# Kernel tuning notes

Measured on AMD Instinct MI355X. Metric: run time of the kernel, lower is better.

The kernel has to match this reference:

```python
import jax, jax.numpy as jnp
import numpy as np
from jax import lax

KSIZE = 3
STRIDE = 1
RATE = 2
FUSE_K = 3
SCALE = 10.0
DN = ('NCHW', 'OIHW', 'NCHW')


def _same_pad_amount(size, k, s):
    out = (size + s - 1) // s
    pad = max(0, (out - 1) * s + k - size)
    return pad // 2, pad - pad // 2


def extract_patches(x, k, s):
    # torch.nn.Unfold with 'same' padding; returns [B, L, C, k, k], L row-major
    B, C, H, W = x.shape
    pt, pb = _same_pad_amount(H, k, s)
    pl, pr = _same_pad_amount(W, k, s)
    xp = jnp.pad(x, ((0, 0), (0, 0), (pt, pb), (pl, pr)))
    Ho = (H + s - 1) // s
    Wo = (W + s - 1) // s
    rows = (jnp.arange(Ho) * s)[:, None] + jnp.arange(k)[None, :]  # [Ho,k]
    cols = (jnp.arange(Wo) * s)[:, None] + jnp.arange(k)[None, :]  # [Wo,k]
    p = xp[:, :, rows, :][:, :, :, :, cols]  # [B,C,Ho,k,Wo,k]
    return p.transpose(0, 2, 4, 1, 3, 5).reshape(B, Ho * Wo, C, k, k)


def setup_inputs() -> dict:
    key = jax.random.key(0)
    kf, kb = jax.random.split(key)
    f = jax.random.normal(kf, (2, 128, 128, 128), dtype=jnp.float32)
    b = jax.random.normal(kb, (2, 128, 128, 128), dtype=jnp.float32)
    mask = jnp.zeros((1, 1, 128, 128), dtype=jnp.float32)  # all patches available
    return {"f": f, "b": b, "mask": mask}


def reference(f, b, mask):
    B, C, Hr, Wr = f.shape
    kernel = 2 * RATE
    # raw background patches for final aggregation: [B, Lb, C, 4, 4]
    raw_w = extract_patches(b, kernel, RATE * STRIDE)
    # nearest downsample by rate (src_idx = i*rate)
    f_ds = f[:, :, ::RATE, ::RATE]
    b_ds = b[:, :, ::RATE, ::RATE]
    Hf, Wf = f_ds.shape[2], f_ds.shape[3]
    Hb, Wb = b_ds.shape[2], b_ds.shape[3]
    L = Hb * Wb
    # matching patches: [B, L, C, 3, 3]
    w = extract_patches(b_ds, KSIZE, STRIDE)
    # mask patches (shared across batch, torch uses m[0])
    m_ds = mask[:, :, ::RATE, ::RATE]
    m = extract_patches(m_ds, KSIZE, STRIDE)[0]  # [L,1,3,3]
    mm = (jnp.mean(m, axis=(1, 2, 3)) == 0.0).astype(f.dtype).reshape(1, L, 1, 1)
    # L2-normalize patch filters (escape_NaN added elementwise before sum, as in torch)
    wn = w / jnp.sqrt(jnp.sum(w * w + 1e-4, axis=(2, 3, 4), keepdims=True))

    def score_one(xi, wi):
        # xi [C,Hf,Wf], wi [L,C,3,3] -> [L,Hf,Wf]
        return lax.conv_general_dilated(xi[None], wi, (1, 1), [(1, 1), (1, 1)],
                                        dimension_numbers=DN)[0]

    y = jax.vmap(score_one)(f_ds, wn)  # [B, L, Hf, Wf]

    # diagonal fuse: identity 3x3 conv on the [L, Hf*Wf] score matrix, twice with transpose
    fw = jnp.eye(FUSE_K, dtype=f.dtype).reshape(1, 1, FUSE_K, FUSE_K)

    def fuse_conv(t):
        return lax.conv_general_dilated(t, fw, (1, 1), [(1, 1), (1, 1)],
                                        dimension_numbers=DN)

    y = y.reshape(B, 1, Hb * Wb, Hf * Wf)
    y = fuse_conv(y).reshape(B, Hb, Wb, Hf, Wf)
    y = y.transpose(0, 2, 1, 4, 3).reshape(B, 1, L, Hf * Wf)
    y = fuse_conv(y).reshape(B, Wb, Hb, Wf, Hf)
    y = y.transpose(0, 2, 1, 4, 3).reshape(B, L, Hf, Wf)

    y = y * mm
    y = jax.nn.softmax(y * SCALE, axis=1) * mm

    def deconv_one(a, wc):
        # conv_transpose2d(a, wc, stride=rate, padding=1); wc [L,C,4,4]
        wt = jnp.flip(wc, (-2, -1)).transpose(1, 0, 2, 3)  # [C,L,4,4]
        pad = kernel - 1 - 1
        return lax.conv_general_dilated(a[None], wt, (1, 1), [(pad, pad), (pad, pad)],
                                        lhs_dilation=(RATE, RATE),
                                        dimension_numbers=DN)[0]

    out = jax.vmap(deconv_one)(y, raw_w) / 4.0  # [B, C, Hr, Wr]
    return out
```

## Files before the change

kernel.cpp:

```cpp
#include <hip/hip_runtime.h>
#include <cstdint>

typedef _Float16 f16x8 __attribute__((ext_vector_type(8)));
typedef float f32x4 __attribute__((ext_vector_type(4)));

typedef __attribute__((address_space(1))) void gvoid;
typedef __attribute__((address_space(3))) void lvoid;

__device__ __forceinline__ void gload16(const void* g, void* l) {
    __builtin_amdgcn_global_load_lds((gvoid*)g, (lvoid*)l, 16, 0, 0);
}

__device__ __forceinline__ void bar() {
    asm volatile("" ::: "memory");
    __builtin_amdgcn_s_barrier();
    asm volatile("" ::: "memory");
}
#define WAITV(N) asm volatile("s_waitcnt vmcnt(" #N ")" ::: "memory")

__global__ __launch_bounds__(256) void downsample_kernel(const float* __restrict__ f,
                                                         const float* __restrict__ b,
                                                         float* __restrict__ fds,
                                                         float* __restrict__ bds) {
    int idx = blockIdx.x * 256 + threadIdx.x;
    const float* src = blockIdx.y ? b : f;
    float* dst = blockIdx.y ? bds : fds;
    int bb = idx >> 19;
    int r = idx & 524287;
    int c = r >> 12, a = (r >> 6) & 63, v = r & 63;
    dst[idx] = src[(size_t)bb * 2097152 + (size_t)c * 16384 + (2 * a) * 128 + 2 * v];
}

__global__ __launch_bounds__(256) void build_mm_kernel(const float* __restrict__ mask,
                                                       float* __restrict__ mm) {
    int l = blockIdx.x * 256 + threadIdx.x;
    if (l >= 4096) return;
    int i = l >> 6, j = l & 63;
    float s = 0.f;
    #pragma unroll
    for (int dy = 0; dy < 3; ++dy)
        #pragma unroll
        for (int dx = 0; dx < 3; ++dx) {
            int a = i + dy - 1, b = j + dx - 1;
            if ((unsigned)a < 64u && (unsigned)b < 64u)
                s += mask[(2 * a) * 128 + 2 * b];
        }
    mm[l] = (s == 0.0f) ? 1.0f : 0.0f;
}

__global__ __launch_bounds__(256) void build_fpatch_kernel(const float* __restrict__ fds,
                                                           _Float16* __restrict__ Fp) {
    int bb = blockIdx.x >> 12;
    int p = blockIdx.x & 4095;
    const float* fb = fds + (size_t)bb * 524288;
    _Float16* Fpb = Fp + (size_t)bb * 4718592;
    int u = p >> 6, v = p & 63;
    for (int k = threadIdx.x; k < 1152; k += 256) {
        int c = k / 9;
        int s = k - 9 * c;
        int dy = s / 3, dx = s - 3 * dy;
        int a = u + dy - 1, bcol = v + dx - 1;
        float val = 0.f;
        if ((unsigned)a < 64u && (unsigned)bcol < 64u)
            val = fb[c * 4096 + a * 64 + bcol];
        Fpb[(size_t)p * 1152 + k] = (_Float16)val;
    }
}

__global__ __launch_bounds__(256) void build_wn_kernel(const float* __restrict__ bds,
                                                       _Float16* __restrict__ Wn) {
    __shared__ float wsh[1152];
    __shared__ float red[4];
    int bb = blockIdx.x >> 12;
    int l = blockIdx.x & 4095;
    const float* bp = bds + (size_t)bb * 524288;
    _Float16* Wnb = Wn + (size_t)bb * 4718592;
    int i = l >> 6, j = l & 63;
    float sq = 0.f;
    for (int k = threadIdx.x; k < 1152; k += 256) {
        int c = k / 9;
        int s = k - 9 * c;
        int dy = s / 3, dx = s - 3 * dy;
        int a = i + dy - 1, bcol = j + dx - 1;
        float val = 0.f;
        if ((unsigned)a < 64u && (unsigned)bcol < 64u)
            val = bp[c * 4096 + a * 64 + bcol];
        wsh[k] = val;
        sq += val * val;
    }
    #pragma unroll
    for (int off = 32; off > 0; off >>= 1) sq += __shfl_xor(sq, off);
    if ((threadIdx.x & 63) == 0) red[threadIdx.x >> 6] = sq;
    __syncthreads();
    float total = red[0] + red[1] + red[2] + red[3] + 0.1152f;
    float rinv = 1.0f / sqrtf(total);
    for (int k = threadIdx.x; k < 1152; k += 256)
        Wnb[(size_t)l * 1152 + k] = (_Float16)(wsh[k] * rinv);
}

__global__ __launch_bounds__(256) void build_vt_kernel(const float* __restrict__ b,
                                                       _Float16* __restrict__ Vt) {
    int bb = blockIdx.x >> 11;
    int n = blockIdx.x & 2047;
    const float* bp = b + (size_t)bb * 2097152;
    _Float16* Vtb = Vt + (size_t)bb * 8388608;
    int c = n >> 4, r = n & 15, rh = r >> 2, rw = r & 3;
    const float* bc = bp + (size_t)c * 16384;
    for (int l = threadIdx.x; l < 4096; l += 256) {
        int lh = l >> 6, lw = l & 63;
        int row = 2 * lh + rh - 1, col = 2 * lw + rw - 1;
        float val = 0.f;
        if ((unsigned)row < 128u && (unsigned)col < 128u)
            val = bc[row * 128 + col];
        Vtb[(size_t)n * 4096 + l] = (_Float16)val;
    }
}

template <int KSTR, int NTILES>
__device__ __forceinline__ void gemm_core(const _Float16* __restrict__ A,
                                          const _Float16* __restrict__ Bt,
                                          _Float16* __restrict__ C,
                                          _Float16* __restrict__ AsB,
                                          _Float16* __restrict__ BsB) {
    const int tid = threadIdx.x;
    const int lane = tid & 63;
    const int wave = tid >> 6;
    const int quad = lane >> 4;
    const int l16 = lane & 15;
    const int wm = wave >> 2;
    const int wn = wave & 3;
    const int bm = blockIdx.y * 256;
    const int bn = blockIdx.x * 256;

    f32x4 acc[8][4] = {};
    f16x8 afr[2][4], bfr[2][4];

    const int s0 = tid, s1 = 512 + tid;
    const int sr0 = s0 >> 2, sr1 = s1 >> 2;
    const int r0 = sr0 ^ ((sr0 >> 2) & 1);
    const int r1 = sr1 ^ ((sr1 >> 2) & 1);
    const int q0 = (s0 & 3) ^ (r0 & 3);
    const int q1 = (s1 & 3) ^ (r1 & 3);
    const int offA0 = (bm + r0) * KSTR + q0 * 8;
    const int offA1 = (bm + r1) * KSTR + q1 * 8;
    const int offB0 = (bn + r0) * KSTR + q0 * 8;
    const int offB1 = (bn + r1) * KSTR + q1 * 8;

#define STAGE_A(buf, kt, kh) do {                                                          \
        gload16(A + offA0 + (kt) * 64 + (kh) * 32, AsB + ((buf) * 2 + (kh)) * 8192 + tid * 8); \
        gload16(A + offA1 + (kt) * 64 + (kh) * 32, AsB + ((buf) * 2 + (kh)) * 8192 + 4096 + tid * 8); \
    } while (0)
#define STAGE_B(buf, kt, kh) do {                                                          \
        gload16(Bt + offB0 + (kt) * 64 + (kh) * 32, BsB + ((buf) * 2 + (kh)) * 8192 + tid * 8); \
        gload16(Bt + offB1 + (kt) * 64 + (kh) * 32, BsB + ((buf) * 2 + (kh)) * 8192 + 4096 + tid * 8); \
    } while (0)

    const int c2 = (l16 >> 2) & 1;
    const int rdoff = ((l16 ^ c2) * 32) + ((quad ^ (l16 & 3)) * 8);

#define LDA(par, buf, kh, mh) do {                                                         \
        _Pragma("unroll")                                                                  \
        for (int mi = 0; mi < 4; ++mi)                                                     \
            afr[par][mi] = *(const f16x8*)&AsB[((buf) * 2 + (kh)) * 8192 +                 \
                (wm * 128 + ((mh) * 4 + mi) * 16) * 32 + rdoff];                           \
    } while (0)
#define LDB(par, buf, kh) do {                                                             \
        _Pragma("unroll")                                                                  \
        for (int ni = 0; ni < 4; ++ni)                                                     \
            bfr[par][ni] = *(const f16x8*)&BsB[((buf) * 2 + (kh)) * 8192 +                 \
                (wn * 64 + ni * 16) * 32 + rdoff];                                         \
    } while (0)
#define MM(apar, bpar, mh) do {                                                            \
        __builtin_amdgcn_s_setprio(1);                                                     \
        _Pragma("unroll")                                                                  \
        for (int mi = 0; mi < 4; ++mi)                                                     \
            _Pragma("unroll")                                                              \
            for (int ni = 0; ni < 4; ++ni)                                                 \
                acc[(mh) * 4 + mi][ni] = __builtin_amdgcn_mfma_f32_16x16x32_f16(           \
                    afr[apar][mi], bfr[bpar][ni], acc[(mh) * 4 + mi][ni], 0, 0, 0);        \
        __builtin_amdgcn_s_setprio(0);                                                     \
    } while (0)

    STAGE_A(0, 0, 0); STAGE_B(0, 0, 0);
    STAGE_A(0, 0, 1); STAGE_B(0, 0, 1);
    STAGE_A(1, 1, 0); STAGE_B(1, 1, 0);
    WAITV(4);
    bar();
    LDA(0, 0, 0, 0); LDB(0, 0, 0);

    #pragma unroll 1
    for (int i = 0; i < NTILES / 2 - 1; ++i) {
        const int t0 = 2 * i;
        STAGE_A(1, t0 + 1, 1); bar();
        LDA(1, 0, 0, 1); MM(0, 0, 0); bar();
        STAGE_B(1, t0 + 1, 1); bar();
        LDA(0, 0, 1, 0); LDB(1, 0, 1); MM(1, 0, 1); bar();
        STAGE_A(0, t0 + 2, 0); bar();
        LDA(1, 0, 1, 1); MM(0, 1, 0); bar();
        STAGE_B(0, t0 + 2, 0); WAITV(4); bar();
        LDA(0, 1, 0, 0); LDB(0, 1, 0); MM(1, 1, 1); bar();
        STAGE_A(0, t0 + 2, 1); bar();
        LDA(1, 1, 0, 1); MM(0, 0, 0); bar();
        STAGE_B(0, t0 + 2, 1); bar();
        LDA(0, 1, 1, 0); LDB(1, 1, 1); MM(1, 0, 1); bar();
        STAGE_A(1, t0 + 3, 0); bar();
        LDA(1, 1, 1, 1); MM(0, 1, 0); bar();
        STAGE_B(1, t0 + 3, 0); WAITV(4); bar();
        LDA(0, 0, 0, 0); LDB(0, 0, 0); MM(1, 1, 1); bar();
    }

    STAGE_A(1, NTILES - 1, 1); bar();
    LDA(1, 0, 0, 1); MM(0, 0, 0); bar();
    STAGE_B(1, NTILES - 1, 1); bar();
    LDA(0, 0, 1, 0); LDB(1, 0, 1); MM(1, 0, 1); bar();
    LDA(1, 0, 1, 1); MM(0, 1, 0); bar();
    WAITV(0); bar();
    LDA(0, 1, 0, 0); LDB(0, 1, 0); MM(1, 1, 1); bar();
    LDA(1, 1, 0, 1); MM(0, 0, 0); bar();
    LDA(0, 1, 1, 0); LDB(1, 1, 1); MM(1, 0, 1); bar();
    LDA(1, 1, 1, 1); MM(0, 1, 0); bar();
    MM(1, 1, 1);

#undef STAGE_A
#undef STAGE_B
#undef LDA
#undef LDB
#undef MM

    #pragma unroll
    for (int mi = 0; mi < 8; ++mi)
        #pragma unroll
        for (int ni = 0; ni < 4; ++ni)
            #pragma unroll
            for (int r = 0; r < 4; ++r) {
                int row = bm + wm * 128 + mi * 16 + quad * 4 + r;
                int col = bn + wn * 64 + ni * 16 + l16;
                C[(size_t)row * 4096 + col] = (_Float16)acc[mi][ni][r];
            }
}

__global__ __launch_bounds__(512, 2) void gemm1_kernel(const _Float16* __restrict__ Fp,
                                                       const _Float16* __restrict__ Wn,
                                                       _Float16* __restrict__ S0) {
    __shared__ __align__(16) _Float16 As[2][2][8192];
    __shared__ __align__(16) _Float16 Bs[2][2][8192];
    const int z = blockIdx.z;
    gemm_core<1152, 18>(Fp + (size_t)z * 4718592, Wn + (size_t)z * 4718592,
                        S0 + (size_t)z * 16777216, &As[0][0][0], &Bs[0][0][0]);
}

__global__ __launch_bounds__(512, 2) void gemm2_kernel(const _Float16* __restrict__ Vt,
                                                       const _Float16* __restrict__ att0,
                                                       const _Float16* __restrict__ att1,
                                                       _Float16* __restrict__ OTh) {
    __shared__ __align__(16) _Float16 As[2][2][8192];
    __shared__ __align__(16) _Float16 Bs[2][2][8192];
    const int z = blockIdx.z;
    gemm_core<4096, 64>(Vt + (size_t)z * 8388608, z ? att1 : att0,
                        OTh + (size_t)z * 8388608, &As[0][0][0], &Bs[0][0][0]);
}

__global__ __launch_bounds__(256) void fuse_softmax_kernel(const _Float16* __restrict__ S0,
                                                           const float* __restrict__ mm,
                                                           _Float16* __restrict__ att0,
                                                           _Float16* __restrict__ att1) {
    __shared__ float red[4];
    const int tid = threadIdx.x;
    const int lane = tid & 63;
    const int wave = tid >> 6;
    int g = blockIdx.x;
    int p_global = ((g & 7) << 10) | (g >> 3);
    const int bb = p_global >> 12;
    const int p = p_global & 4095;
    const _Float16* S = S0 + (size_t)bb * 16777216;
    _Float16* att = bb ? att1 : att0;
    const int pbase = ((p & 63) << 6) | (p >> 6);

    float acc[16];
    #pragma unroll
    for (int k = 0; k < 16; ++k) acc[k] = 0.f;

    #pragma unroll
    for (int t2 = -1; t2 <= 1; ++t2) {
        int b2 = pbase + t2;
        if ((unsigned)b2 >= 4096u) continue;
        int pp = ((b2 & 63) << 6) | (b2 >> 6);
        #pragma unroll
        for (int t1 = -1; t1 <= 1; ++t1) {
            int rr = pp + t1;
            if ((unsigned)rr >= 4096u) continue;
            const _Float16* row = S + (size_t)rr * 4096;
            #pragma unroll
            for (int k = 0; k < 16; ++k) {
                int l = k * 256 + tid;
                int i = (k * 256 + wave * 64) >> 6;
                int it2 = i + t2;
                if (it2 >= 0 && it2 < 64) {
                    int c = l + t2 * 64 + t1;
                    if ((unsigned)c < 4096u)
                        acc[k] += (float)row[c];
                } else if (it2 == 64) {
                    if (lane <= 62) {
                        int c = lane + 1 + t1;
                        if ((unsigned)c < 4096u) acc[k] += (float)row[c];
                    }
                } else {
                    if (lane >= 1) {
                        int c = 4031 + lane + t1;
                        if ((unsigned)c < 4096u) acc[k] += (float)row[c];
                    }
                }
            }
        }
    }

    float mv[16];
    float lmax = -1e30f;
    #pragma unroll
    for (int k = 0; k < 16; ++k) {
        int l = k * 256 + tid;
        mv[k] = mm[l];
        float lg = acc[k] * mv[k] * 10.0f;
        acc[k] = lg;
        lmax = fmaxf(lmax, lg);
    }
    #pragma unroll
    for (int off = 32; off > 0; off >>= 1) lmax = fmaxf(lmax, __shfl_xor(lmax, off));
    if (lane == 0) red[wave] = lmax;
    __syncthreads();
    lmax = fmaxf(fmaxf(red[0], red[1]), fmaxf(red[2], red[3]));
    __syncthreads();

    float lsum = 0.f;
    #pragma unroll
    for (int k = 0; k < 16; ++k) {
        float e = __expf(acc[k] - lmax);
        acc[k] = e;
        lsum += e;
    }
    #pragma unroll
    for (int off = 32; off > 0; off >>= 1) lsum += __shfl_xor(lsum, off);
    if (lane == 0) red[wave] = lsum;
    __syncthreads();
    float inv = 1.0f / (red[0] + red[1] + red[2] + red[3]);
    #pragma unroll
    for (int k = 0; k < 16; ++k) {
        int l = k * 256 + tid;
        att[(size_t)p * 4096 + l] = (_Float16)(acc[k] * inv * mv[k]);
    }
}

__global__ __launch_bounds__(256) void assemble_kernel(const _Float16* __restrict__ OTh,
                                                       float* __restrict__ out) {
    int idx = blockIdx.x * 256 + threadIdx.x;
    int bb = idx >> 21;
    int w = idx & 2097151;
    const _Float16* OTb = OTh + (size_t)bb * 8388608;
    int x = w & 127, y = (w >> 7) & 127, c = w >> 14;
    int r0 = (y + 1) & 1, s0 = (x + 1) & 1;
    float acc = 0.f;
    #pragma unroll
    for (int a = 0; a < 2; ++a) {
        int rh = r0 + 2 * a;
        int ph = (y + 1 - rh) >> 1;
        if ((unsigned)ph < 64u) {
            #pragma unroll
            for (int bq = 0; bq < 2; ++bq) {
                int rw = s0 + 2 * bq;
                int pw = (x + 1 - rw) >> 1;
                if ((unsigned)pw < 64u)
                    acc += (float)OTb[(size_t)(c * 16 + rh * 4 + rw) * 4096 + ph * 64 + pw];
            }
        }
    }
    out[idx] = 0.25f * acc;
}

extern "C" void kernel_launch(void* const* d_in, const int* in_sizes, int n_in,
                              void* d_out, int out_size, void* d_ws, size_t ws_size,
                              hipStream_t stream) {
    const float* f = (const float*)d_in[0];
    const float* b = (const float*)d_in[1];
    const float* mask = (const float*)d_in[2];
    float* out = (float*)d_out;
    char* ws = (char*)d_ws;

    float* mm = (float*)ws;
    _Float16* Fp = (_Float16*)(ws + 16384);
    _Float16* Wn = (_Float16*)(ws + 16384 + 18874368);
    _Float16* att0 = (_Float16*)(ws + 16384);
    _Float16* S0 = (_Float16*)(ws + 37765120);
    _Float16* Vt = (_Float16*)(ws + 37765120);
    _Float16* OTh = (_Float16*)(ws + 37765120 + 33554432);
    float* fds = (float*)(ws + 104873984);
    float* bds = (float*)(ws + 104873984 + 4194304);
    _Float16* att1 = (_Float16*)(ws + 104873984);

    downsample_kernel<<<dim3(4096, 2), 256, 0, stream>>>(f, b, fds, bds);
    build_mm_kernel<<<16, 256, 0, stream>>>(mask, mm);
    build_fpatch_kernel<<<8192, 256, 0, stream>>>(fds, Fp);
    build_wn_kernel<<<8192, 256, 0, stream>>>(bds, Wn);

    gemm1_kernel<<<dim3(16, 16, 2), 512, 0, stream>>>(Fp, Wn, S0);
    fuse_softmax_kernel<<<8192, 256, 0, stream>>>(S0, mm, att0, att1);

    build_vt_kernel<<<4096, 256, 0, stream>>>(b, Vt);
    gemm2_kernel<<<dim3(16, 8, 2), 512, 0, stream>>>(Vt, att0, att1, OTh);
    assemble_kernel<<<16384, 256, 0, stream>>>(OTh, out);
}
```

Before: 431.1 us.

## Replace double-buffered register fragments with single-buffered loads and explicit LDS waits

```diff
diff --git a/kernel.cpp b/kernel.cpp
--- a/kernel.cpp
+++ b/kernel.cpp
@@ -17,6 +17,8 @@
     asm volatile("" ::: "memory");
 }
 #define WAITV(N) asm volatile("s_waitcnt vmcnt(" #N ")" ::: "memory")
+#define WAITL0 do { asm volatile("s_waitcnt lgkmcnt(0)" ::: "memory"); \
+                    __builtin_amdgcn_sched_barrier(0); } while (0)
 
 __global__ __launch_bounds__(256) void downsample_kernel(const float* __restrict__ f,
                                                          const float* __restrict__ b,
@@ -133,7 +135,6 @@
     const int bn = blockIdx.x * 256;
 
     f32x4 acc[8][4] = {};
-    f16x8 afr[2][4], bfr[2][4];
 
     const int s0 = tid, s1 = 512 + tid;
     const int sr0 = s0 >> 2, sr1 = s1 >> 2;
@@ -158,74 +159,72 @@
     const int c2 = (l16 >> 2) & 1;
     const int rdoff = ((l16 ^ c2) * 32) + ((quad ^ (l16 & 3)) * 8);
 
-#define LDA(par, buf, kh, mh) do {                                                         \
-        _Pragma("unroll")                                                                  \
-        for (int mi = 0; mi < 4; ++mi)                                                     \
-            afr[par][mi] = *(const f16x8*)&AsB[((buf) * 2 + (kh)) * 8192 +                 \
-                (wm * 128 + ((mh) * 4 + mi) * 16) * 32 + rdoff];                           \
-    } while (0)
-#define LDB(par, buf, kh) do {                                                             \
-        _Pragma("unroll")                                                                  \
-        for (int ni = 0; ni < 4; ++ni)                                                     \
-            bfr[par][ni] = *(const f16x8*)&BsB[((buf) * 2 + (kh)) * 8192 +                 \
-                (wn * 64 + ni * 16) * 32 + rdoff];                                         \
-    } while (0)
-#define MM(apar, bpar, mh) do {                                                            \
-        __builtin_amdgcn_s_setprio(1);                                                     \
-        _Pragma("unroll")                                                                  \
-        for (int mi = 0; mi < 4; ++mi)                                                     \
-            _Pragma("unroll")                                                              \
-            for (int ni = 0; ni < 4; ++ni)                                                 \
-                acc[(mh) * 4 + mi][ni] = __builtin_amdgcn_mfma_f32_16x16x32_f16(           \
-                    afr[apar][mi], bfr[bpar][ni], acc[(mh) * 4 + mi][ni], 0, 0, 0);        \
-        __builtin_amdgcn_s_setprio(0);                                                     \
-    } while (0)
+    f16x8 afr[4], bfr[4];
+    auto LDA = [&](int buf, int kh, int mh) {
+        #pragma unroll
+        for (int mi = 0; mi < 4; ++mi)
+            afr[mi] = *(const f16x8*)&AsB[((buf) * 2 + (kh)) * 8192 +
+                                          (wm * 128 + ((mh) * 4 + mi) * 16) * 32 + rdoff];
+    };
+    auto LDB = [&](int buf, int kh) {
+        #pragma unroll
+        for (int ni = 0; ni < 4; ++ni)
+            bfr[ni] = *(const f16x8*)&BsB[((buf) * 2 + (kh)) * 8192 +
+                                          (wn * 64 + ni * 16) * 32 + rdoff];
+    };
+    auto MM = [&](int mh) {
+        __builtin_amdgcn_s_setprio(1);
+        #pragma unroll
+        for (int mi = 0; mi < 4; ++mi)
+            #pragma unroll
+            for (int ni = 0; ni < 4; ++ni)
+                acc[mh * 4 + mi][ni] = __builtin_amdgcn_mfma_f32_16x16x32_f16(
+                    afr[mi], bfr[ni], acc[mh * 4 + mi][ni], 0, 0, 0);
+        __builtin_amdgcn_s_setprio(0);
+    };
 
     STAGE_A(0, 0, 0); STAGE_B(0, 0, 0);
     STAGE_A(0, 0, 1); STAGE_B(0, 0, 1);
     STAGE_A(1, 1, 0); STAGE_B(1, 1, 0);
     WAITV(4);
     bar();
-    LDA(0, 0, 0, 0); LDB(0, 0, 0);
 
     #pragma unroll 1
     for (int i = 0; i < NTILES / 2 - 1; ++i) {
         const int t0 = 2 * i;
-        STAGE_A(1, t0 + 1, 1); bar();
-        LDA(1, 0, 0, 1); MM(0, 0, 0); bar();
-        STAGE_B(1, t0 + 1, 1); bar();
-        LDA(0, 0, 1, 0); LDB(1, 0, 1); MM(1, 0, 1); bar();
-        STAGE_A(0, t0 + 2, 0); bar();
-        LDA(1, 0, 1, 1); MM(0, 1, 0); bar();
-        STAGE_B(0, t0 + 2, 0); WAITV(4); bar();
-        LDA(0, 1, 0, 0); LDB(0, 1, 0); MM(1, 1, 1); bar();
-        STAGE_A(0, t0 + 2, 1); bar();
-        LDA(1, 1, 0, 1); MM(0, 0, 0); bar();
-        STAGE_B(0, t0 + 2, 1); bar();
-        LDA(0, 1, 1, 0); LDB(1, 1, 1); MM(1, 0, 1); bar();
-        STAGE_A(1, t0 + 3, 0); bar();
-        LDA(1, 1, 1, 1); MM(0, 1, 0); bar();
-        STAGE_B(1, t0 + 3, 0); WAITV(4); bar();
-        LDA(0, 0, 0, 0); LDB(0, 0, 0); MM(1, 1, 1); bar();
-    }
-
-    STAGE_A(1, NTILES - 1, 1); bar();
-    LDA(1, 0, 0, 1); MM(0, 0, 0); bar();
-    STAGE_B(1, NTILES - 1, 1); bar();
-    LDA(0, 0, 1, 0); LDB(1, 0, 1); MM(1, 0, 1); bar();
-    LDA(1, 0, 1, 1); MM(0, 1, 0); bar();
-    WAITV(0); bar();
-    LDA(0, 1, 0, 0); LDB(0, 1, 0); MM(1, 1, 1); bar();
-    LDA(1, 1, 0, 1); MM(0, 0, 0); bar();
-    LDA(0, 1, 1, 0); LDB(1, 1, 1); MM(1, 0, 1); bar();
-    LDA(1, 1, 1, 1); MM(0, 1, 0); bar();
-    MM(1, 1, 1);
+        LDA(0, 0, 0); LDB(0, 0); STAGE_A(1, t0 + 1, 1);
+        bar(); WAITL0; MM(0); bar();
+        LDA(0, 0, 1); STAGE_B(1, t0 + 1, 1);
+        bar(); WAITL0; MM(1); bar();
+        LDA(0, 1, 0); LDB(0, 1); STAGE_A(0, t0 + 2, 0);
+        bar(); WAITL0; MM(0); bar();
+        LDA(0, 1, 1); STAGE_B(0, t0 + 2, 0); WAITV(4);
+        bar(); WAITL0; MM(1); bar();
+        LDA(1, 0, 0); LDB(1, 0); STAGE_A(0, t0 + 2, 1);
+        bar(); WAITL0; MM(0); bar();
+        LDA(1, 0, 1); STAGE_B(0, t0 + 2, 1);
+        bar(); WAITL0; MM(1); bar();
+        LDA(1, 1, 0); LDB(1, 1); STAGE_A(1, t0 + 3, 0);
+        bar(); WAITL0; MM(0); bar();
+        LDA(1, 1, 1); STAGE_B(1, t0 + 3, 0); WAITV(4);
+        bar(); WAITL0; MM(1); bar();
+    }
+
+    LDA(0, 0, 0); LDB(0, 0); STAGE_A(1, NTILES - 1, 1);
+    bar(); WAITL0; MM(0); bar();
+    LDA(0, 0, 1); STAGE_B(1, NTILES - 1, 1);
+    bar(); WAITL0; MM(1); bar();
+    LDA(0, 1, 0); LDB(0, 1);
+    bar(); WAITL0; MM(0); bar();
+    LDA(0, 1, 1);
+    bar(); WAITL0; MM(1); WAITV(0); bar();
+    LDA(1, 0, 0); LDB(1, 0); bar(); WAITL0; MM(0); bar();
+    LDA(1, 0, 1);            bar(); WAITL0; MM(1); bar();
+    LDA(1, 1, 0); LDB(1, 1); bar(); WAITL0; MM(0); bar();
+    LDA(1, 1, 1);            bar(); WAITL0; MM(1);
 
 #undef STAGE_A
 #undef STAGE_B
-#undef LDA
-#undef LDB
-#undef MM
 
     #pragma unroll
     for (int mi = 0; mi < 8; ++mi)
```

After: 433.2 us. Within noise of the previous version (+0.5%).

## Load GEMM B fragments directly from global memory into registers, drop B LDS staging

Applied to the files above, without the earlier changes.

```diff
diff --git a/kernel.cpp b/kernel.cpp
--- a/kernel.cpp
+++ b/kernel.cpp
@@ -120,8 +120,7 @@
 __device__ __forceinline__ void gemm_core(const _Float16* __restrict__ A,
                                           const _Float16* __restrict__ Bt,
                                           _Float16* __restrict__ C,
-                                          _Float16* __restrict__ AsB,
-                                          _Float16* __restrict__ BsB) {
+                                          _Float16* __restrict__ AsB) {
     const int tid = threadIdx.x;
     const int lane = tid & 63;
     const int wave = tid >> 6;
@@ -133,7 +132,6 @@
     const int bn = blockIdx.x * 256;
 
     f32x4 acc[8][4] = {};
-    f16x8 afr[2][4], bfr[2][4];
 
     const int s0 = tid, s1 = 512 + tid;
     const int sr0 = s0 >> 2, sr1 = s1 >> 2;
@@ -143,87 +141,88 @@
     const int q1 = (s1 & 3) ^ (r1 & 3);
     const int offA0 = (bm + r0) * KSTR + q0 * 8;
     const int offA1 = (bm + r1) * KSTR + q1 * 8;
-    const int offB0 = (bn + r0) * KSTR + q0 * 8;
-    const int offB1 = (bn + r1) * KSTR + q1 * 8;
-
-#define STAGE_A(buf, kt, kh) do {                                                          \
+
+#define STAGE(buf, kt, kh) do {                                                            \
         gload16(A + offA0 + (kt) * 64 + (kh) * 32, AsB + ((buf) * 2 + (kh)) * 8192 + tid * 8); \
         gload16(A + offA1 + (kt) * 64 + (kh) * 32, AsB + ((buf) * 2 + (kh)) * 8192 + 4096 + tid * 8); \
     } while (0)
-#define STAGE_B(buf, kt, kh) do {                                                          \
-        gload16(Bt + offB0 + (kt) * 64 + (kh) * 32, BsB + ((buf) * 2 + (kh)) * 8192 + tid * 8); \
-        gload16(Bt + offB1 + (kt) * 64 + (kh) * 32, BsB + ((buf) * 2 + (kh)) * 8192 + 4096 + tid * 8); \
-    } while (0)
 
     const int c2 = (l16 >> 2) & 1;
     const int rdoff = ((l16 ^ c2) * 32) + ((quad ^ (l16 & 3)) * 8);
 
-#define LDA(par, buf, kh, mh) do {                                                         \
-        _Pragma("unroll")                                                                  \
-        for (int mi = 0; mi < 4; ++mi)                                                     \
-            afr[par][mi] = *(const f16x8*)&AsB[((buf) * 2 + (kh)) * 8192 +                 \
-                (wm * 128 + ((mh) * 4 + mi) * 16) * 32 + rdoff];                           \
-    } while (0)
-#define LDB(par, buf, kh) do {                                                             \
+    f16x8 afr[4], bfr0[4], bfr1[4];
+    const _Float16* bB = Bt + (size_t)(bn + wn * 64 + l16) * KSTR + quad * 8;
+
+#define LDB(dst, kt, kc) do {                                                              \
         _Pragma("unroll")                                                                  \
         for (int ni = 0; ni < 4; ++ni)                                                     \
-            bfr[par][ni] = *(const f16x8*)&BsB[((buf) * 2 + (kh)) * 8192 +                 \
-                (wn * 64 + ni * 16) * 32 + rdoff];                                         \
+            dst[ni] = *(const f16x8*)(bB + (size_t)ni * 16 * KSTR + (kt) * 64 + (kc) * 32); \
+        __builtin_amdgcn_sched_barrier(0);                                                 \
     } while (0)
-#define MM(apar, bpar, mh) do {                                                            \
+
+    auto LDA = [&](int buf, int kh, int mh) {
+        #pragma unroll
+        for (int mi = 0; mi < 4; ++mi)
+            afr[mi] = *(const f16x8*)&AsB[((buf) * 2 + (kh)) * 8192 +
+                                          (wm * 128 + ((mh) * 4 + mi) * 16) * 32 + rdoff];
+    };
+#define MM(bf, mh) do {                                                                    \
         __builtin_amdgcn_s_setprio(1);                                                     \
         _Pragma("unroll")                                                                  \
         for (int mi = 0; mi < 4; ++mi)                                                     \
             _Pragma("unroll")                                                              \
             for (int ni = 0; ni < 4; ++ni)                                                 \
                 acc[(mh) * 4 + mi][ni] = __builtin_amdgcn_mfma_f32_16x16x32_f16(           \
-                    afr[apar][mi], bfr[bpar][ni], acc[(mh) * 4 + mi][ni], 0, 0, 0);        \
+                    afr[mi], bf[ni], acc[(mh) * 4 + mi][ni], 0, 0, 0);                     \
         __builtin_amdgcn_s_setprio(0);                                                     \
     } while (0)
 
-    STAGE_A(0, 0, 0); STAGE_B(0, 0, 0);
-    STAGE_A(0, 0, 1); STAGE_B(0, 0, 1);
-    STAGE_A(1, 1, 0); STAGE_B(1, 1, 0);
+    LDB(bfr0, 0, 0);
+    STAGE(0, 0, 0);
+    STAGE(0, 0, 1);
+    STAGE(1, 1, 0);
     WAITV(4);
     bar();
-    LDA(0, 0, 0, 0); LDB(0, 0, 0);
 
     #pragma unroll 1
     for (int i = 0; i < NTILES / 2 - 1; ++i) {
         const int t0 = 2 * i;
-        STAGE_A(1, t0 + 1, 1); bar();
-        LDA(1, 0, 0, 1); MM(0, 0, 0); bar();
-        STAGE_B(1, t0 + 1, 1); bar();
-        LDA(0, 0, 1, 0); LDB(1, 0, 1); MM(1, 0, 1); bar();
-        STAGE_A(0, t0 + 2, 0); bar();
-        LDA(1, 0, 1, 1); MM(0, 1, 0); bar();
-        STAGE_B(0, t0 + 2, 0); WAITV(4); bar();
-        LDA(0, 1, 0, 0); LDB(0, 1, 0); MM(1, 1, 1); bar();
-        STAGE_A(0, t0 + 2, 1); bar();
-        LDA(1, 1, 0, 1); MM(0, 0, 0); bar();
-        STAGE_B(0, t0 + 2, 1); bar();
-        LDA(0, 1, 1, 0); LDB(1, 1, 1); MM(1, 0, 1); bar();
-        STAGE_A(1, t0 + 3, 0); bar();
-        LDA(1, 1, 1, 1); MM(0, 1, 0); bar();
-        STAGE_B(1, t0 + 3, 0); WAITV(4); bar();
-        LDA(0, 0, 0, 0); LDB(0, 0, 0); MM(1, 1, 1); bar();
-    }
-
-    STAGE_A(1, NTILES - 1, 1); bar();
-    LDA(1, 0, 0, 1); MM(0, 0, 0); bar();
-    STAGE_B(1, NTILES - 1, 1); bar();
-    LDA(0, 0, 1, 0); LDB(1, 0, 1); MM(1, 0, 1); bar();
-    LDA(1, 0, 1, 1); MM(0, 1, 0); bar();
-    WAITV(0); bar();
-    LDA(0, 1, 0, 0); LDB(0, 1, 0); MM(1, 1, 1); bar();
-    LDA(1, 1, 0, 1); MM(0, 0, 0); bar();
-    LDA(0, 1, 1, 0); LDB(1, 1, 1); MM(1, 0, 1); bar();
-    LDA(1, 1, 1, 1); MM(0, 1, 0); bar();
-    MM(1, 1, 1);
-
-#undef STAGE_A
-#undef STAGE_B
-#undef LDA
+        LDB(bfr1, t0, 1); STAGE(1, t0 + 1, 1); LDA(0, 0, 0); WAITV(6);
+        bar(); MM(bfr0, 0); bar();
+        LDA(0, 0, 1);
+        bar(); MM(bfr0, 1); bar();
+        LDB(bfr0, t0 + 1, 0); STAGE(0, t0 + 2, 0); LDA(0, 1, 0); WAITV(8);
+        bar(); MM(bfr1, 0); bar();
+        LDA(0, 1, 1);
+        bar(); MM(bfr1, 1); bar();
+        LDB(bfr1, t0 + 1, 1); STAGE(0, t0 + 2, 1); LDA(1, 0, 0); WAITV(8);
+        bar(); MM(bfr0, 0); bar();
+        LDA(1, 0, 1);
+        bar(); MM(bfr0, 1); bar();
+        LDB(bfr0, t0 + 2, 0); STAGE(1, t0 + 3, 0); LDA(1, 1, 0); WAITV(8);
+        bar(); MM(bfr1, 0); bar();
+        LDA(1, 1, 1);
+        bar(); MM(bfr1, 1); bar();
+    }
+
+    LDB(bfr1, NTILES - 2, 1); STAGE(1, NTILES - 1, 1); LDA(0, 0, 0); WAITV(8);
+    bar(); MM(bfr0, 0); bar();
+    LDA(0, 0, 1);
+    bar(); MM(bfr0, 1); bar();
+    LDB(bfr0, NTILES - 1, 0); LDA(0, 1, 0); WAITV(6);
+    bar(); MM(bfr1, 0); bar();
+    LDA(0, 1, 1);
+    bar(); MM(bfr1, 1); bar();
+    LDB(bfr1, NTILES - 1, 1); LDA(1, 0, 0); WAITV(4);
+    bar(); MM(bfr0, 0); bar();
+    LDA(1, 0, 1);
+    bar(); MM(bfr0, 1); bar();
+    LDA(1, 1, 0); WAITV(0);
+    bar(); MM(bfr1, 0); bar();
+    LDA(1, 1, 1);
+    bar(); MM(bfr1, 1);
+
+#undef STAGE
 #undef LDB
 #undef MM
 
@@ -243,10 +242,9 @@
                                                        const _Float16* __restrict__ Wn,
                                                        _Float16* __restrict__ S0) {
     __shared__ __align__(16) _Float16 As[2][2][8192];
-    __shared__ __align__(16) _Float16 Bs[2][2][8192];
     const int z = blockIdx.z;
     gemm_core<1152, 18>(Fp + (size_t)z * 4718592, Wn + (size_t)z * 4718592,
-                        S0 + (size_t)z * 16777216, &As[0][0][0], &Bs[0][0][0]);
+                        S0 + (size_t)z * 16777216, &As[0][0][0]);
 }
 
 __global__ __launch_bounds__(512, 2) void gemm2_kernel(const _Float16* __restrict__ Vt,
@@ -254,10 +252,9 @@
                                                        const _Float16* __restrict__ att1,
                                                        _Float16* __restrict__ OTh) {
     __shared__ __align__(16) _Float16 As[2][2][8192];
-    __shared__ __align__(16) _Float16 Bs[2][2][8192];
     const int z = blockIdx.z;
     gemm_core<4096, 64>(Vt + (size_t)z * 8388608, z ? att1 : att0,
-                        OTh + (size_t)z * 8388608, &As[0][0][0], &Bs[0][0][0]);
+                        OTh + (size_t)z * 8388608, &As[0][0][0]);
 }
 
 __global__ __launch_bounds__(256) void fuse_softmax_kernel(const _Float16* __restrict__ S0,
```

New measurement: 526.1 us. 22.0% more time.
